# Performance work log

Measured on AMD Instinct MI355X. Metric: run time of the kernel, lower is better.

## Reference

```python
import jax, jax.numpy as jnp
import numpy as np

B, S, D, H = 2, 2048, 1024, 16
HD = D // H  # head_dim = 64


def _rope(t, cos, sin):
    # t: (B, H, S, HD); cos/sin: (S, HD//2) -> rotate interleaved pairs
    t2 = t.reshape(*t.shape[:-1], HD // 2, 2)
    t1, t2_ = t2[..., 0], t2[..., 1]
    c = cos[None, None, :, :]
    s = sin[None, None, :, :]
    out = jnp.stack([t1 * c - t2_ * s, t1 * s + t2_ * c], axis=-1)
    return out.reshape(t.shape)


def setup_inputs() -> dict:
    key = jax.random.key(0)
    ks = jax.random.split(key, 5)
    x = jax.random.normal(ks[0], (B, S, D), dtype=jnp.float32)
    attn_mask = jnp.tril(jnp.ones((S, S), dtype=bool))  # causal
    # standard RoPE angles: pos * inv_freq
    inv_freq = 1.0 / (10000.0 ** (jnp.arange(0, HD, 2, dtype=jnp.float32) / HD))
    freqs = jnp.arange(S, dtype=jnp.float32)[:, None] * inv_freq[None, :]  # (S, HD//2)
    std = 1.0 / np.sqrt(D)
    w_qkv = jax.random.normal(ks[1], (3 * D, D), dtype=jnp.float32) * std
    b_qkv = jnp.zeros((3 * D,), dtype=jnp.float32)
    w_proj = jax.random.normal(ks[2], (D, D), dtype=jnp.float32) * std
    b_proj = jnp.zeros((D,), dtype=jnp.float32)
    return {"x": x, "attn_mask": attn_mask, "freqs": freqs,
            "w_qkv": w_qkv, "b_qkv": b_qkv, "w_proj": w_proj, "b_proj": b_proj}


def reference(x, attn_mask, freqs, w_qkv, b_qkv, w_proj, b_proj):
    # QKV projection: (B,S,D) -> (B,S,3D), split per einops pattern (three, H, HD)
    qkv = x @ w_qkv.T + b_qkv
    qkv = qkv.reshape(B, S, 3, H, HD)
    q = jnp.transpose(qkv[:, :, 0], (0, 2, 1, 3))  # (B,H,S,HD)
    k = jnp.transpose(qkv[:, :, 1], (0, 2, 1, 3))
    v = jnp.transpose(qkv[:, :, 2], (0, 2, 1, 3))
    cos, sin = jnp.cos(freqs), jnp.sin(freqs)
    q = _rope(q, cos, sin)
    k = _rope(k, cos, sin)
    scale = 1.0 / np.sqrt(HD)
    scores = jnp.einsum("bhqd,bhkd->bhqk", q, k) * scale  # (B,H,S,S)
    scores = jnp.where(attn_mask[None, None, :, :], scores, jnp.finfo(scores.dtype).min)
    attn = jax.nn.softmax(scores, axis=-1)
    out = jnp.einsum("bhqk,bhkd->bhqd", attn, v)  # (B,H,S,HD)
    out = jnp.transpose(out, (0, 2, 1, 3)).reshape(B, S, D)
    return out @ w_proj.T + b_proj
```

## Files before the change

### kernel.cpp

```cpp
#include <hip/hip_runtime.h>

#define S_LEN 2048
#define NH 16
#define HD 64
#define DMODEL 1024

typedef __bf16 bf16x8 __attribute__((ext_vector_type(8)));
typedef float floatx4 __attribute__((ext_vector_type(4)));
typedef short short8 __attribute__((ext_vector_type(8)));

__device__ inline unsigned short f2bf(float f) {
    union { float f; unsigned u; } v; v.f = f;
    unsigned u = v.u;
    unsigned r = (u + 0x7FFFu + ((u >> 16) & 1u)) >> 16;
    return (unsigned short)r;
}

__device__ __forceinline__ void gload_lds16(const void* g, void* l) {
    __builtin_amdgcn_global_load_lds(
        (const __attribute__((address_space(1))) unsigned int*)g,
        (__attribute__((address_space(3))) unsigned int*)l, 16, 0, 0);
}

__device__ __forceinline__ void cvt4(const float4* __restrict__ src,
                                     uint2* __restrict__ dst, int i) {
    float4 v = src[i];
    union { unsigned short u[4]; uint2 d; } o;
    o.u[0] = f2bf(v.x); o.u[1] = f2bf(v.y); o.u[2] = f2bf(v.z); o.u[3] = f2bf(v.w);
    dst[i] = o.d;
}

__global__ __launch_bounds__(256) void prep_kernel(
    const float* __restrict__ x, const float* __restrict__ wq,
    const float* __restrict__ wp, const float* __restrict__ freqs,
    unsigned short* __restrict__ xb, unsigned short* __restrict__ wqb,
    unsigned short* __restrict__ wpb, float2* __restrict__ cs)
{
    const int tid = blockIdx.x * 256 + threadIdx.x;
    const int nth = gridDim.x * 256;
    for (int i = tid; i < (4096 * 1024) / 4; i += nth) cvt4((const float4*)x, (uint2*)xb, i);
    for (int i = tid; i < (3072 * 1024) / 4; i += nth) cvt4((const float4*)wq, (uint2*)wqb, i);
    for (int i = tid; i < (1024 * 1024) / 4; i += nth) cvt4((const float4*)wp, (uint2*)wpb, i);
    for (int i = tid; i < S_LEN * 32; i += nth) {
        const float f = freqs[i];
        float2 c; c.x = cosf(f); c.y = sinf(f);
        cs[i] = c;
    }
}

#define SROW(r) (((r) & 3) ^ (((r) >> 2) & 3))

#define QKV_STAGE(dA, dB, kk) do { \
    gload_lds16(ag + (kk),               (dA) + wv * 512); \
    gload_lds16(ag + 64 * DMODEL + (kk), (dA) + 2048 + wv * 512); \
    gload_lds16(bg + (kk),               (dB) + wv * 512); \
    gload_lds16(bg + 64 * DMODEL + (kk), (dB) + 2048 + wv * 512); \
} while (0)

#define QKV_COMPUTE(sA, sB) do { \
    bf16x8 af[4]; \
    _Pragma("unroll") for (int m_ = 0; m_ < 4; m_++) af[m_] = *(const bf16x8*)&(sA)[aoff[m_]]; \
    _Pragma("unroll") for (int n_ = 0; n_ < 4; n_++) { \
        bf16x8 bf = *(const bf16x8*)&(sB)[boff[n_]]; \
        _Pragma("unroll") for (int m_ = 0; m_ < 4; m_++) \
            acc[m_][n_] = __builtin_amdgcn_mfma_f32_16x16x32_bf16(af[m_], bf, acc[m_][n_], 0, 0, 0); \
    } \
} while (0)

__global__ __launch_bounds__(256, 3) void qkv_gemm_kernel(
    const unsigned short* __restrict__ xb, const unsigned short* __restrict__ wqb,
    const float* __restrict__ bias, const float2* __restrict__ cs,
    unsigned short* __restrict__ qb, unsigned short* __restrict__ kb,
    unsigned short* __restrict__ vb)
{
    __shared__ __align__(16) unsigned short smem[16384];
    unsigned short* A0 = smem;
    unsigned short* B0 = smem + 4096;
    unsigned short* A1 = smem + 8192;
    unsigned short* B1 = smem + 12288;

    const int t = threadIdx.x;
    const int v = (blockIdx.x & 7) * 96 + (blockIdx.x >> 3);
    const int mbase = (v / 24) * 128;
    const int nbase = (v % 24) * 128;
    const int wv = t >> 6, lane = t & 63;
    const int quad = lane >> 4, l16 = lane & 15;
    const int wr = wv >> 1, wc = wv & 1;

    floatx4 acc[4][4];
    #pragma unroll
    for (int m = 0; m < 4; m++)
        #pragma unroll
        for (int n = 0; n < 4; n++)
            #pragma unroll
            for (int r = 0; r < 4; r++) acc[m][n][r] = 0.f;

    const int srow = t >> 2;
    const int schunk = (t & 3) ^ SROW(srow);
    const unsigned short* ag = xb + (size_t)(mbase + srow) * DMODEL + schunk * 8;
    const unsigned short* bg = wqb + (size_t)(nbase + srow) * DMODEL + schunk * 8;

    const int Sl = SROW(l16);
    int aoff[4], boff[4];
    #pragma unroll
    for (int m = 0; m < 4; m++) aoff[m] = (wr * 64 + m * 16 + l16) * 32 + (quad ^ Sl) * 8;
    #pragma unroll
    for (int n = 0; n < 4; n++) boff[n] = (wc * 64 + n * 16 + l16) * 32 + (quad ^ Sl) * 8;

    QKV_STAGE(A0, B0, 0);
    __syncthreads();
    for (int k0 = 0; k0 < DMODEL; k0 += 64) {
        QKV_STAGE(A1, B1, k0 + 32);
        QKV_COMPUTE(A0, B0);
        __syncthreads();
        if (k0 + 64 < DMODEL) QKV_STAGE(A0, B0, k0 + 64);
        QKV_COMPUTE(A1, B1);
        __syncthreads();
    }

    const int part = nbase >> 10;
    const int bidx = mbase >> 11;
    const int s0   = mbase & 2047;

    if (part == 2) {
        unsigned short* Vt = smem;
        const int hb = (nbase & 1023) >> 6;
        float bvv[4];
        #pragma unroll
        for (int nt = 0; nt < 4; nt++) bvv[nt] = bias[nbase + wc * 64 + nt * 16 + l16];
        #pragma unroll
        for (int shalf = 0; shalf < 2; shalf++) {
            __syncthreads();
            if (wr == shalf) {
                #pragma unroll
                for (int nt = 0; nt < 4; nt++) {
                    const int hdl = wc * 64 + nt * 16 + l16;
                    #pragma unroll
                    for (int m = 0; m < 4; m++)
                        #pragma unroll
                        for (int r = 0; r < 4; r++)
                            Vt[hdl * 72 + m * 16 + quad * 4 + r] = f2bf(acc[m][nt][r] + bvv[nt]);
                }
            }
            __syncthreads();
            const int hdl = t & 127, sp = t >> 7;
            const size_t bh2 = (size_t)bidx * NH + hb + (hdl >> 6);
            #pragma unroll
            for (int c = 0; c < 4; c++) {
                const int sl0 = (sp * 4 + c) * 8;
                const int sg = s0 + shalf * 64 + sl0;
                short8 vv = *(const short8*)&Vt[hdl * 72 + sl0];
                *(short8*)&vb[((bh2 * 256 + (sg >> 3)) * 64 + (hdl & 63)) * 8] = vv;
            }
        }
    } else {
        const size_t bhb = (size_t)bidx * NH;
        const int odd = l16 & 1;
        #pragma unroll
        for (int nt = 0; nt < 4; nt++) {
            const int n_ = nbase + wc * 64 + nt * 16 + l16;
            const int hd = n_ & 63;
            const size_t bh = bhb + ((n_ & 1023) >> 6);
            const float bvv = bias[n_];
            const int ci = (nt * 16 + l16) >> 1;
            #pragma unroll
            for (int m = 0; m < 4; m++) {
                #pragma unroll
                for (int r = 0; r < 4; r++) {
                    const int s = s0 + wr * 64 + m * 16 + quad * 4 + r;
                    float val = acc[m][nt][r] + bvv;
                    float other = __shfl_xor(val, 1, 64);
                    const float2 csv = cs[(size_t)s * 32 + ci];
                    float outv = odd ? fmaf(other, csv.y, val * csv.x)
                                     : fmaf(-other, csv.y, val * csv.x);
                    if (part == 0) {
                        qb[(bh * S_LEN + s) * HD + hd] = f2bf(outv * 0.125f);
                    } else {
                        kb[((bh * 8 + (hd >> 3)) * (size_t)S_LEN + s) * 8 + (hd & 7)] = f2bf(outv);
                    }
                }
            }
        }
    }
}

__global__ __launch_bounds__(256, 3) void attn_kernel(
    const unsigned short* __restrict__ qb, const unsigned short* __restrict__ kb,
    const unsigned short* __restrict__ vbk, unsigned short* __restrict__ ao)
{
    __shared__ __align__(16) unsigned short Ks[2][8 * 512];
    __shared__ __align__(16) unsigned short Vt[2][8 * 512];
    __shared__ __align__(16) unsigned short Pw[4][16 * 72];

    const int t = threadIdx.x;
    const int wv = t >> 6, lane = t & 63, quad = lane >> 4, l16 = lane & 15;
    const int qt   = 31 - (blockIdx.x >> 5);
    const int bhid = blockIdx.x & 31;
    const int h = bhid & 15, b = bhid >> 4;
    const size_t bh = (size_t)b * NH + h;
    const unsigned short* qg  = qb + bh * S_LEN * HD;
    const unsigned short* kgB = kb + bh * 8 * S_LEN * 8;
    const unsigned short* vgB = vbk + bh * 256 * 64 * 8;

    bf16x8 qf[2];
    {
        const unsigned short* q0 = qg + (size_t)(qt * 64 + wv * 16 + l16) * HD;
        qf[0] = *(const bf16x8*)&q0[quad * 8];
        qf[1] = *(const bf16x8*)&q0[32 + quad * 8];
    }

    bf16x8 ones;
    {
        union { short8 s; bf16x8 v; } o;
        for (int j = 0; j < 8; j++) o.s[j] = 0x3F80;
        ones = o.v;
    }

    floatx4 lfr = {0.f, 0.f, 0.f, 0.f};
    floatx4 Ofr[4];
    for (int nt = 0; nt < 4; nt++)
        for (int r = 0; r < 4; r++) Ofr[nt][r] = 0.f;

    const int ntiles = qt + 1;

#define ATTN_STAGE(bufi, kt_) do { \
    const int kb_ = (kt_) * 64; \
    const unsigned short* g0 = kgB + ((size_t)(2 * wv) * S_LEN + kb_ + lane) * 8; \
    gload_lds16(g0,             &Ks[bufi][(2 * wv) * 512]); \
    gload_lds16(g0 + S_LEN * 8, &Ks[bufi][(2 * wv + 1) * 512]); \
    const unsigned short* g1 = vgB + ((size_t)((kb_ >> 3) + 2 * wv) * 64 + lane) * 8; \
    gload_lds16(g1,          &Vt[bufi][(2 * wv) * 512]); \
    gload_lds16(g1 + 64 * 8, &Vt[bufi][(2 * wv + 1) * 512]); \
} while (0)

#define ATTN_COMPUTE(bufi, kt_) do { \
    const int kbase = (kt_) * 64; \
    float pex[4][4]; \
    _Pragma("unroll") for (int sub = 0; sub < 4; sub++) { \
        bf16x8 kf0 = *(const bf16x8*)&Ks[bufi][(0 * 4 + quad) * 512 + (sub * 16 + l16) * 8]; \
        bf16x8 kf1 = *(const bf16x8*)&Ks[bufi][(1 * 4 + quad) * 512 + (sub * 16 + l16) * 8]; \
        floatx4 sacc = {0.f, 0.f, 0.f, 0.f}; \
        sacc = __builtin_amdgcn_mfma_f32_16x16x32_bf16(kf0, qf[0], sacc, 0, 0, 0); \
        sacc = __builtin_amdgcn_mfma_f32_16x16x32_bf16(kf1, qf[1], sacc, 0, 0, 0); \
        _Pragma("unroll") for (int r = 0; r < 4; r++) pex[sub][r] = sacc[r]; \
    } \
    if ((kt_) == qt) { \
        const int q = qt * 64 + wv * 16 + l16; \
        _Pragma("unroll") for (int sub = 0; sub < 4; sub++) \
            _Pragma("unroll") for (int r = 0; r < 4; r++) { \
                const int key = kbase + sub * 16 + quad * 4 + r; \
                if (key > q) pex[sub][r] = -1e30f; \
            } \
    } \
    _Pragma("unroll") for (int sub = 0; sub < 4; sub++) { \
        union { unsigned short s[4]; uint2 u; } pk; \
        _Pragma("unroll") for (int r = 0; r < 4; r++) pk.s[r] = f2bf(__expf(pex[sub][r])); \
        *(uint2*)&Pw[wv][l16 * 72 + sub * 16 + quad * 4] = pk.u; \
    } \
    { \
        bf16x8 pf0 = *(const bf16x8*)&Pw[wv][l16 * 72 + quad * 8]; \
        bf16x8 pf1 = *(const bf16x8*)&Pw[wv][l16 * 72 + 32 + quad * 8]; \
        lfr = __builtin_amdgcn_mfma_f32_16x16x32_bf16(ones, pf0, lfr, 0, 0, 0); \
        lfr = __builtin_amdgcn_mfma_f32_16x16x32_bf16(ones, pf1, lfr, 0, 0, 0); \
        _Pragma("unroll") for (int nt = 0; nt < 4; nt++) { \
            bf16x8 v0 = *(const bf16x8*)&Vt[bufi][(0 * 4 + quad) * 512 + (nt * 16 + l16) * 8]; \
            bf16x8 v1 = *(const bf16x8*)&Vt[bufi][(1 * 4 + quad) * 512 + (nt * 16 + l16) * 8]; \
            Ofr[nt] = __builtin_amdgcn_mfma_f32_16x16x32_bf16(pf0, v0, Ofr[nt], 0, 0, 0); \
            Ofr[nt] = __builtin_amdgcn_mfma_f32_16x16x32_bf16(pf1, v1, Ofr[nt], 0, 0, 0); \
        } \
    } \
} while (0)

    ATTN_STAGE(0, 0);
    __syncthreads();
    for (int kt = 0; kt < ntiles; ) {
        if (kt + 1 < ntiles) ATTN_STAGE(1, kt + 1);
        ATTN_COMPUTE(0, kt);
        kt++;
        if (kt >= ntiles) break;
        __syncthreads();
        if (kt + 1 < ntiles) ATTN_STAGE(0, kt + 1);
        ATTN_COMPUTE(1, kt);
        kt++;
        if (kt >= ntiles) break;
        __syncthreads();
    }

    float linv[4];
    #pragma unroll
    for (int r = 0; r < 4; r++) {
        float lq = __shfl(lfr[0], (lane & 48) | (quad * 4 + r), 64);
        linv[r] = 1.f / lq;
    }
    #pragma unroll
    for (int nt = 0; nt < 4; nt++)
        #pragma unroll
        for (int r = 0; r < 4; r++) {
            const int s = qt * 64 + wv * 16 + quad * 4 + r;
            ao[((size_t)b * S_LEN + s) * DMODEL + h * HD + nt * 16 + l16] =
                f2bf(Ofr[nt][r] * linv[r]);
        }
#undef ATTN_STAGE
#undef ATTN_COMPUTE
}

#define PROJ_STAGE(dA, dB, kk) do { \
    gload_lds16(ag + (kk),               (dA) + wv * 512); \
    gload_lds16(ag + 64 * DMODEL + (kk), (dA) + 2048 + wv * 512); \
    gload_lds16(bg + (kk),               (dB) + wv * 512); \
} while (0)

#define PROJ_COMPUTE(sA, sB) do { \
    bf16x8 af[4]; \
    _Pragma("unroll") for (int m_ = 0; m_ < 4; m_++) af[m_] = *(const bf16x8*)&(sA)[aoff[m_]]; \
    _Pragma("unroll") for (int n_ = 0; n_ < 2; n_++) { \
        bf16x8 bf = *(const bf16x8*)&(sB)[boff[n_]]; \
        _Pragma("unroll") for (int m_ = 0; m_ < 4; m_++) \
            acc[m_][n_] = __builtin_amdgcn_mfma_f32_16x16x32_bf16(af[m_], bf, acc[m_][n_], 0, 0, 0); \
    } \
} while (0)

__global__ __launch_bounds__(256, 3) void proj_kernel(
    const unsigned short* __restrict__ a, const unsigned short* __restrict__ wpb,
    const float* __restrict__ bias, float* __restrict__ out)
{
    __shared__ __align__(16) unsigned short smem[12288];
    unsigned short* A0 = smem;
    unsigned short* B0 = smem + 4096;
    unsigned short* A1 = smem + 6144;
    unsigned short* B1 = smem + 10240;

    const int t = threadIdx.x;
    const int v = (blockIdx.x & 7) * 64 + (blockIdx.x >> 3);
    const int mbase = (v >> 4) * 128;
    const int nbase = (v & 15) * 64;
    const int wv = t >> 6, lane = t & 63, quad = lane >> 4, l16 = lane & 15;
    const int wr = wv >> 1, wc = wv & 1;

    floatx4 acc[4][2];
    #pragma unroll
    for (int m = 0; m < 4; m++)
        #pragma unroll
        for (int n = 0; n < 2; n++)
            #pragma unroll
            for (int r = 0; r < 4; r++) acc[m][n][r] = 0.f;

    const int srow = t >> 2;
    const int schunk = (t & 3) ^ SROW(srow);
    const unsigned short* ag = a + (size_t)(mbase + srow) * DMODEL + schunk * 8;
    const unsigned short* bg = wpb + (size_t)(nbase + srow) * DMODEL + schunk * 8;

    const int Sl = SROW(l16);
    int aoff[4], boff[2];
    #pragma unroll
    for (int m = 0; m < 4; m++) aoff[m] = (wr * 64 + m * 16 + l16) * 32 + (quad ^ Sl) * 8;
    #pragma unroll
    for (int n = 0; n < 2; n++) boff[n] = (wc * 32 + n * 16 + l16) * 32 + (quad ^ Sl) * 8;

    PROJ_STAGE(A0, B0, 0);
    __syncthreads();
    for (int k0 = 0; k0 < DMODEL; k0 += 64) {
        PROJ_STAGE(A1, B1, k0 + 32);
        PROJ_COMPUTE(A0, B0);
        __syncthreads();
        if (k0 + 64 < DMODEL) PROJ_STAGE(A0, B0, k0 + 64);
        PROJ_COMPUTE(A1, B1);
        __syncthreads();
    }

    #pragma unroll
    for (int n = 0; n < 2; n++) {
        const int nn = nbase + wc * 32 + n * 16 + l16;
        const float bvv = bias[nn];
        #pragma unroll
        for (int m = 0; m < 4; m++)
            #pragma unroll
            for (int r = 0; r < 4; r++)
                out[(size_t)(mbase + wr * 64 + m * 16 + quad * 4 + r) * DMODEL + nn] =
                    acc[m][n][r] + bvv;
    }
}

extern "C" void kernel_launch(void* const* d_in, const int* in_sizes, int n_in,
                              void* d_out, int out_size, void* d_ws, size_t ws_size,
                              hipStream_t stream) {
    const float* x      = (const float*)d_in[0];
    const float* freqs  = (const float*)d_in[2];
    const float* w_qkv  = (const float*)d_in[3];
    const float* b_qkv  = (const float*)d_in[4];
    const float* w_proj = (const float*)d_in[5];
    const float* b_proj = (const float*)d_in[6];
    float* out = (float*)d_out;

    unsigned short* ws = (unsigned short*)d_ws;
    const size_t HSZ = (size_t)2 * NH * S_LEN * HD;
    unsigned short* qb  = ws;
    unsigned short* kb  = ws + HSZ;
    unsigned short* vb  = ws + 2 * HSZ;
    unsigned short* ao  = ws + 3 * HSZ;
    unsigned short* xb  = ws + 4 * HSZ;
    unsigned short* wqb = xb + (size_t)4096 * 1024;
    unsigned short* wpb = wqb + (size_t)3072 * 1024;
    float2* cs = (float2*)(wpb + (size_t)1024 * 1024);

    prep_kernel<<<2048, 256, 0, stream>>>(x, w_qkv, w_proj, freqs, xb, wqb, wpb, cs);
    qkv_gemm_kernel<<<768, 256, 0, stream>>>(xb, wqb, b_qkv, cs, qb, kb, vb);
    attn_kernel<<<1024, 256, 0, stream>>>(qb, kb, vb, ao);
    proj_kernel<<<512, 256, 0, stream>>>(ao, wpb, b_proj, out);
}
```

Baseline: 192.3 us.

## Deepen GEMM LDS pipeline to four buffers with explicit vmcnt waits

Both the QKV and output-projection GEMMs move from a double-buffered LDS scheme with __syncthreads to a four-slot ring. Loads are issued two k-steps ahead, and each step ends in an inline s_waitcnt vmcnt(N) plus s_barrier, so only the oldest stage has to land before compute. The aim is to hide global-to-LDS latency and cut barrier stalls. The cost is double the shared memory per block and a lower occupancy hint for the QKV kernel (launch bounds 3 to 2 blocks). The hand-written waitcnt values depend on the exact count of outstanding loads per stage.

```diff
diff --git a/kernel.cpp b/kernel.cpp
--- a/kernel.cpp
+++ b/kernel.cpp
@@ -21,6 +21,11 @@
         (const __attribute__((address_space(1))) unsigned int*)g,
         (__attribute__((address_space(3))) unsigned int*)l, 16, 0, 0);
 }
+
+#define WAITV_BAR(N) do { \
+    asm volatile("s_waitcnt vmcnt(" #N ")\n\ts_barrier" ::: "memory"); \
+    __builtin_amdgcn_sched_barrier(0); \
+} while (0)
 
 __device__ __forceinline__ void cvt4(const float4* __restrict__ src,
                                      uint2* __restrict__ dst, int i) {
@@ -50,34 +55,34 @@
 
 #define SROW(r) (((r) & 3) ^ (((r) >> 2) & 3))
 
-#define QKV_STAGE(dA, dB, kk) do { \
-    gload_lds16(ag + (kk),               (dA) + wv * 512); \
-    gload_lds16(ag + 64 * DMODEL + (kk), (dA) + 2048 + wv * 512); \
-    gload_lds16(bg + (kk),               (dB) + wv * 512); \
-    gload_lds16(bg + 64 * DMODEL + (kk), (dB) + 2048 + wv * 512); \
-} while (0)
-
-#define QKV_COMPUTE(sA, sB) do { \
+#define QKV_STAGE(bi, kk) do { \
+    unsigned short* dA_ = smem + (bi) * 8192; \
+    unsigned short* dB_ = dA_ + 4096; \
+    gload_lds16(ag + (kk),               dA_ + wv * 512); \
+    gload_lds16(ag + 64 * DMODEL + (kk), dA_ + 2048 + wv * 512); \
+    gload_lds16(bg + (kk),               dB_ + wv * 512); \
+    gload_lds16(bg + 64 * DMODEL + (kk), dB_ + 2048 + wv * 512); \
+} while (0)
+
+#define QKV_COMPUTE(bi) do { \
+    const unsigned short* sA_ = smem + (bi) * 8192; \
+    const unsigned short* sB_ = sA_ + 4096; \
     bf16x8 af[4]; \
-    _Pragma("unroll") for (int m_ = 0; m_ < 4; m_++) af[m_] = *(const bf16x8*)&(sA)[aoff[m_]]; \
+    _Pragma("unroll") for (int m_ = 0; m_ < 4; m_++) af[m_] = *(const bf16x8*)&sA_[aoff[m_]]; \
     _Pragma("unroll") for (int n_ = 0; n_ < 4; n_++) { \
-        bf16x8 bf = *(const bf16x8*)&(sB)[boff[n_]]; \
+        bf16x8 bf = *(const bf16x8*)&sB_[boff[n_]]; \
         _Pragma("unroll") for (int m_ = 0; m_ < 4; m_++) \
             acc[m_][n_] = __builtin_amdgcn_mfma_f32_16x16x32_bf16(af[m_], bf, acc[m_][n_], 0, 0, 0); \
     } \
 } while (0)
 
-__global__ __launch_bounds__(256, 3) void qkv_gemm_kernel(
+__global__ __launch_bounds__(256, 2) void qkv_gemm_kernel(
     const unsigned short* __restrict__ xb, const unsigned short* __restrict__ wqb,
     const float* __restrict__ bias, const float2* __restrict__ cs,
     unsigned short* __restrict__ qb, unsigned short* __restrict__ kb,
     unsigned short* __restrict__ vb)
 {
-    __shared__ __align__(16) unsigned short smem[16384];
-    unsigned short* A0 = smem;
-    unsigned short* B0 = smem + 4096;
-    unsigned short* A1 = smem + 8192;
-    unsigned short* B1 = smem + 12288;
+    __shared__ __align__(16) unsigned short smem[32768];
 
     const int t = threadIdx.x;
     const int v = (blockIdx.x & 7) * 96 + (blockIdx.x >> 3);
@@ -107,16 +112,18 @@
     #pragma unroll
     for (int n = 0; n < 4; n++) boff[n] = (wc * 64 + n * 16 + l16) * 32 + (quad ^ Sl) * 8;
 
-    QKV_STAGE(A0, B0, 0);
-    __syncthreads();
-    for (int k0 = 0; k0 < DMODEL; k0 += 64) {
-        QKV_STAGE(A1, B1, k0 + 32);
-        QKV_COMPUTE(A0, B0);
-        __syncthreads();
-        if (k0 + 64 < DMODEL) QKV_STAGE(A0, B0, k0 + 64);
-        QKV_COMPUTE(A1, B1);
-        __syncthreads();
-    }
+    QKV_STAGE(0, 0);
+    QKV_STAGE(1, 32);
+    #pragma unroll 4
+    for (int tt = 0; tt < 28; tt++) {
+        QKV_STAGE((tt + 2) & 3, (tt + 2) * 32);
+        WAITV_BAR(8);
+        QKV_COMPUTE(tt & 3);
+    }
+    QKV_STAGE(2, 30 * 32); WAITV_BAR(8); QKV_COMPUTE(0);
+    QKV_STAGE(3, 31 * 32); WAITV_BAR(8); QKV_COMPUTE(1);
+    WAITV_BAR(4); QKV_COMPUTE(2);
+    WAITV_BAR(0); QKV_COMPUTE(3);
 
     const int part = nbase >> 10;
     const int bidx = mbase >> 11;
@@ -304,17 +311,21 @@
 #undef ATTN_COMPUTE
 }
 
-#define PROJ_STAGE(dA, dB, kk) do { \
-    gload_lds16(ag + (kk),               (dA) + wv * 512); \
-    gload_lds16(ag + 64 * DMODEL + (kk), (dA) + 2048 + wv * 512); \
-    gload_lds16(bg + (kk),               (dB) + wv * 512); \
-} while (0)
-
-#define PROJ_COMPUTE(sA, sB) do { \
+#define PROJ_STAGE(bi, kk) do { \
+    unsigned short* dA_ = smem + (bi) * 6144; \
+    unsigned short* dB_ = dA_ + 4096; \
+    gload_lds16(ag + (kk),               dA_ + wv * 512); \
+    gload_lds16(ag + 64 * DMODEL + (kk), dA_ + 2048 + wv * 512); \
+    gload_lds16(bg + (kk),               dB_ + wv * 512); \
+} while (0)
+
+#define PROJ_COMPUTE(bi) do { \
+    const unsigned short* sA_ = smem + (bi) * 6144; \
+    const unsigned short* sB_ = sA_ + 4096; \
     bf16x8 af[4]; \
-    _Pragma("unroll") for (int m_ = 0; m_ < 4; m_++) af[m_] = *(const bf16x8*)&(sA)[aoff[m_]]; \
+    _Pragma("unroll") for (int m_ = 0; m_ < 4; m_++) af[m_] = *(const bf16x8*)&sA_[aoff[m_]]; \
     _Pragma("unroll") for (int n_ = 0; n_ < 2; n_++) { \
-        bf16x8 bf = *(const bf16x8*)&(sB)[boff[n_]]; \
+        bf16x8 bf = *(const bf16x8*)&sB_[boff[n_]]; \
         _Pragma("unroll") for (int m_ = 0; m_ < 4; m_++) \
             acc[m_][n_] = __builtin_amdgcn_mfma_f32_16x16x32_bf16(af[m_], bf, acc[m_][n_], 0, 0, 0); \
     } \
@@ -324,11 +335,7 @@
     const unsigned short* __restrict__ a, const unsigned short* __restrict__ wpb,
     const float* __restrict__ bias, float* __restrict__ out)
 {
-    __shared__ __align__(16) unsigned short smem[12288];
-    unsigned short* A0 = smem;
-    unsigned short* B0 = smem + 4096;
-    unsigned short* A1 = smem + 6144;
-    unsigned short* B1 = smem + 10240;
+    __shared__ __align__(16) unsigned short smem[24576];
 
     const int t = threadIdx.x;
     const int v = (blockIdx.x & 7) * 64 + (blockIdx.x >> 3);
@@ -357,16 +364,18 @@
     #pragma unroll
     for (int n = 0; n < 2; n++) boff[n] = (wc * 32 + n * 16 + l16) * 32 + (quad ^ Sl) * 8;
 
-    PROJ_STAGE(A0, B0, 0);
-    __syncthreads();
-    for (int k0 = 0; k0 < DMODEL; k0 += 64) {
-        PROJ_STAGE(A1, B1, k0 + 32);
-        PROJ_COMPUTE(A0, B0);
-        __syncthreads();
-        if (k0 + 64 < DMODEL) PROJ_STAGE(A0, B0, k0 + 64);
-        PROJ_COMPUTE(A1, B1);
-        __syncthreads();
-    }
+    PROJ_STAGE(0, 0);
+    PROJ_STAGE(1, 32);
+    #pragma unroll 4
+    for (int tt = 0; tt < 28; tt++) {
+        PROJ_STAGE((tt + 2) & 3, (tt + 2) * 32);
+        WAITV_BAR(6);
+        PROJ_COMPUTE(tt & 3);
+    }
+    PROJ_STAGE(2, 30 * 32); WAITV_BAR(6); PROJ_COMPUTE(0);
+    PROJ_STAGE(3, 31 * 32); WAITV_BAR(6); PROJ_COMPUTE(1);
+    WAITV_BAR(3); PROJ_COMPUTE(2);
+    WAITV_BAR(0); PROJ_COMPUTE(3);
 
     #pragma unroll
     for (int n = 0; n < 2; n++) {
```

Result: slower. 198.3 us (+3.1%).
